# Performance work log

Hardware: AMD Instinct MI355X
Metric: run time of the kernel (lower is better)

## Reference

```python
import jax, jax.numpy as jnp
import numpy as np

NUM_EMBEDDINGS = 1024
EMBEDDING_DIM = 256
COMMITMENT_COST = 0.25


def setup_inputs() -> dict:
    key = jax.random.key(0)
    k1, k2 = jax.random.split(key)
    inputs = jax.random.normal(k1, (64, 1024, EMBEDDING_DIM), dtype=jnp.float32)
    # codebook initialized uniform(-1/K, 1/K) as in the torch module
    embedding = jax.random.uniform(
        k2, (NUM_EMBEDDINGS, EMBEDDING_DIM), dtype=jnp.float32,
        minval=-1.0 / NUM_EMBEDDINGS, maxval=1.0 / NUM_EMBEDDINGS)
    return {"inputs": inputs, "embedding": embedding}


def reference(inputs, embedding):
    # flatten to [N, D]
    D = embedding.shape[1]
    flat = inputs.reshape(-1, D)
    distances = (jnp.sum(flat * flat, axis=1, keepdims=True)
                 + jnp.sum(embedding * embedding, axis=1)
                 - 2.0 * jnp.matmul(flat, embedding.T))
    encoding_indices = jnp.argmin(distances, axis=1)  # [N]
    # one_hot @ embedding == gather; use gather (same math, no NxK one-hot)
    quantized = jnp.take(embedding, encoding_indices, axis=0).reshape(inputs.shape)
    # commitment loss: mse(stop_grad(quantized), inputs)
    e_latent_loss = jnp.mean(jnp.square(jax.lax.stop_gradient(quantized) - inputs))
    loss = COMMITMENT_COST * e_latent_loss
    # straight-through estimator
    quantized = inputs + jax.lax.stop_gradient(quantized - inputs)
    return quantized, loss, encoding_indices.reshape(inputs.shape[:-1])
```

## Files before the change

### kernel.cpp

```cpp
#include <hip/hip_runtime.h>
#include <cfloat>
#include <climits>

#define N_ROWS 65536
#define DIM 256
#define K_CODES 1024
#define N_ELEM 16777216
#define OUT_LOSS_OFF 16777216
#define OUT_IDX_OFF  16777217

#define ROWS_PB 128
#define CT 128
#define EPS_MARGIN 1.5e-4f
#define SHORTLIST_EPS 6e-4f
#define RB 8

#define WS_PARTIALS 0
#define WS_ESQ      8192
#define WS_IDX      12288
#define WS_FLAGCNT  274432
#define WS_FLAGLIST 274436
#define WS_EHI      540672
#define WS_ELO      1064960
#define WS_EHIT     1589248

typedef unsigned short u16;
typedef __attribute__((ext_vector_type(8))) short bf16x8;
typedef __attribute__((ext_vector_type(4))) float f32x4;

__device__ __forceinline__ void glds16(const u16* g, u16* l) {
    __builtin_amdgcn_global_load_lds(
        (const __attribute__((address_space(1))) unsigned int*)(const void*)g,
        (__attribute__((address_space(3))) unsigned int*)(void*)l,
        16, 0, 0);
}

__device__ __forceinline__ void bsplit(float x, u16& h, u16& l) {
    unsigned u = __float_as_uint(x);
    unsigned hb = (u + 0x7fffu + ((u >> 16) & 1u)) >> 16;
    h = (u16)hb;
    float hf = __uint_as_float(hb << 16);
    float lf = x - hf;
    unsigned u2 = __float_as_uint(lf);
    l = (u16)((u2 + 0x7fffu + ((u2 >> 16) & 1u)) >> 16);
}

__device__ __forceinline__ float np_pairwise_sumsq(const float* __restrict__ a) {
    float half[2];
    #pragma unroll
    for (int h = 0; h < 2; ++h) {
        const float* p = a + h * 128;
        float r[8];
        #pragma unroll
        for (int j = 0; j < 8; ++j) r[j] = __fmul_rn(p[j], p[j]);
        for (int i = 8; i < 128; i += 8) {
            #pragma unroll
            for (int j = 0; j < 8; ++j)
                r[j] = __fadd_rn(r[j], __fmul_rn(p[i + j], p[i + j]));
        }
        half[h] = __fadd_rn(__fadd_rn(__fadd_rn(r[0], r[1]), __fadd_rn(r[2], r[3])),
                            __fadd_rn(__fadd_rn(r[4], r[5]), __fadd_rn(r[6], r[7])));
    }
    return __fadd_rn(half[0], half[1]);
}

__global__ void xsplit_kernel(const float* __restrict__ x, u16* __restrict__ xhi,
                              u16* __restrict__ xlo) {
    int i4 = blockIdx.x * 256 + threadIdx.x;
    float4 v = ((const float4*)x)[i4];
    ushort4 h, l;
    bsplit(v.x, h.x, l.x); bsplit(v.y, h.y, l.y);
    bsplit(v.z, h.z, l.z); bsplit(v.w, h.w, l.w);
    ((ushort4*)xhi)[i4] = h;
    ((ushort4*)xlo)[i4] = l;
}

__global__ void esplit_kernel(const float* __restrict__ e, u16* __restrict__ ehi,
                              u16* __restrict__ elo, u16* __restrict__ ehiT) {
    int i4 = blockIdx.x * 256 + threadIdx.x;
    float4 v = ((const float4*)e)[i4];
    ushort4 h, l;
    bsplit(v.x, h.x, l.x); bsplit(v.y, h.y, l.y);
    bsplit(v.z, h.z, l.z); bsplit(v.w, h.w, l.w);
    ((ushort4*)ehi)[i4] = h;
    ((ushort4*)elo)[i4] = l;
    int c = i4 >> 6;
    int f4 = i4 & 63;
    int qid = f4 >> 1;
    ((ushort4*)ehiT)[((size_t)qid * 1024 + c) * 2 + (f4 & 1)] = h;
}

__global__ void esq_kernel(const float* __restrict__ e, float* __restrict__ esq) {
    int c = blockIdx.x * 256 + threadIdx.x;
    if (c < K_CODES) esq[c] = np_pairwise_sumsq(e + c * DIM);
}

__launch_bounds__(512, 4)
__global__ void argmin_kernel(const u16* __restrict__ xhi, const u16* __restrict__ xlo,
                              const u16* __restrict__ ehi, const u16* __restrict__ elo,
                              const float* __restrict__ esq, int* __restrict__ wsIdx,
                              int* __restrict__ flagCnt, int* __restrict__ flagList) {
    __shared__ __align__(16) unsigned char lds[65536];
    __shared__ float esq_s[CT];
    u16* xhiS = (u16*)lds;
    u16* xloS = (u16*)(lds + 16384);
    u16* ehiS = (u16*)(lds + 32768);
    u16* eloS = (u16*)(lds + 49152);

    const int t = threadIdx.x;
    const int w = t >> 6;
    const int l = t & 63;
    const int lane15 = l & 15;
    const int quad = l >> 4;
    const int rowBase = blockIdx.x * ROWS_PB;
    const int wr = w >> 1;
    const int wc = w & 1;

    float bv[8], sv[8]; int bi[8];
    #pragma unroll
    for (int i = 0; i < 8; ++i) { bv[i] = FLT_MAX; sv[i] = FLT_MAX; bi[i] = INT_MAX; }

    const int arr = w & 3;
    const int half = w >> 2;
    const u16* src; u16* dst; int gIsX;
    if (arr == 0)      { src = xhi; dst = xhiS; gIsX = 1; }
    else if (arr == 1) { src = xlo; dst = xloS; gIsX = 1; }
    else if (arr == 2) { src = ehi; dst = ehiS; gIsX = 0; }
    else               { src = elo; dst = eloS; gIsX = 0; }
    const int sub = l >> 3;
    const int jb = l & 7;
    const int sb = jb ^ sub;

    for (int ct = 0; ct < 8; ++ct) {
        const int ctBase = ct * CT;
        __syncthreads();
        if (t < CT) esq_s[t] = esq[ctBase + t];

        f32x4 acc[2][4];
        #pragma unroll
        for (int ti = 0; ti < 2; ++ti)
            #pragma unroll
            for (int tj = 0; tj < 4; ++tj) acc[ti][tj] = (f32x4){0.f, 0.f, 0.f, 0.f};

        for (int ch = 0; ch < 4; ++ch) {
            __syncthreads();
            const int gRowBase = gIsX ? rowBase : ctBase;
            #pragma unroll
            for (int i = 0; i < 8; ++i) {
                int r = half * 64 + i * 8 + sub;
                glds16(src + (size_t)(gRowBase + r) * 256 + ch * 64 + sb * 8,
                       dst + half * 4096 + i * 512);
            }
            __syncthreads();

            #pragma unroll
            for (int kk = 0; kk < 2; ++kk) {
                bf16x8 ah[2], al4[2], bh[4], bl[4];
                const int blk = kk * 4 + quad;
                #pragma unroll
                for (int ti = 0; ti < 2; ++ti) {
                    int r = wr * 32 + ti * 16 + lane15;
                    int off = r * 64 + ((blk ^ (r & 7)) * 8);
                    ah[ti]  = *(const bf16x8*)(xhiS + off);
                    al4[ti] = *(const bf16x8*)(xloS + off);
                }
                #pragma unroll
                for (int tj = 0; tj < 4; ++tj) {
                    int r = wc * 64 + tj * 16 + lane15;
                    int off = r * 64 + ((blk ^ (r & 7)) * 8);
                    bh[tj] = *(const bf16x8*)(ehiS + off);
                    bl[tj] = *(const bf16x8*)(eloS + off);
                }
                #pragma unroll
                for (int ti = 0; ti < 2; ++ti)
                    #pragma unroll
                    for (int tj = 0; tj < 4; ++tj) {
                        acc[ti][tj] = __builtin_amdgcn_mfma_f32_16x16x32_bf16(al4[ti], bh[tj], acc[ti][tj], 0, 0, 0);
                        acc[ti][tj] = __builtin_amdgcn_mfma_f32_16x16x32_bf16(ah[ti], bl[tj], acc[ti][tj], 0, 0, 0);
                        acc[ti][tj] = __builtin_amdgcn_mfma_f32_16x16x32_bf16(ah[ti], bh[tj], acc[ti][tj], 0, 0, 0);
                    }
            }
        }

        #pragma unroll
        for (int tj = 0; tj < 4; ++tj) {
            int cLoc = wc * 64 + tj * 16 + lane15;
            float cs = esq_s[cLoc];
            int c = ctBase + cLoc;
            #pragma unroll
            for (int ti = 0; ti < 2; ++ti)
                #pragma unroll
                for (int r4 = 0; r4 < 4; ++r4) {
                    int slot = ti * 4 + r4;
                    float s = fmaf(-2.0f, acc[ti][tj][r4], cs);
                    if (s < bv[slot]) {
                        sv[slot] = bv[slot]; bv[slot] = s; bi[slot] = c;
                    } else if (s < sv[slot]) {
                        sv[slot] = s;
                    }
                }
        }
    }

    __syncthreads();
    float* bvA = (float*)lds;
    float* svA = (float*)(lds + 16896);
    int*   biA = (int*)(lds + 33792);
    const int contrib = wc * 16 + lane15;
    #pragma unroll
    for (int slot = 0; slot < 8; ++slot) {
        int m = wr * 32 + (slot >> 2) * 16 + quad * 4 + (slot & 3);
        bvA[m * 33 + contrib] = bv[slot];
        svA[m * 33 + contrib] = sv[slot];
        biA[m * 33 + contrib] = bi[slot];
    }
    __syncthreads();

    if (t < ROWS_PB) {
        float bb = FLT_MAX, ss = FLT_MAX;
        int ii = INT_MAX;
        for (int k = 0; k < 32; ++k) {
            float v  = bvA[t * 33 + k];
            int   id = biA[t * 33 + k];
            float s2 = svA[t * 33 + k];
            if (v < bb || (v == bb && id < ii)) {
                ss = fminf(bb, s2);
                bb = v; ii = id;
            } else {
                ss = fminf(ss, v);
            }
        }
        int row = rowBase + t;
        wsIdx[row] = ii;
        if (ss - bb < EPS_MARGIN) {
            int p = atomicAdd(flagCnt, 1);
            flagList[p] = row;
        }
    }
}

__launch_bounds__(256)
__global__ void rescore_kernel(const float* __restrict__ x, const float* __restrict__ e,
                               const u16* __restrict__ ehiT, const float* __restrict__ esq,
                               int* __restrict__ wsIdx, const int* __restrict__ flagCnt,
                               const int* __restrict__ flagList) {
    __shared__ __align__(16) float xsh[RB][DIM];
    __shared__ float Ash[RB];
    __shared__ float minsh[RB][256];
    __shared__ float thrsh[RB];
    __shared__ int scnt[RB];
    __shared__ int slist[RB][32];
    __shared__ float sres[RB][32];
    const int t = threadIdx.x;
    const int cnt = *flagCnt;
    const int ngroups = (cnt + RB - 1) / RB;
    for (int g = blockIdx.x; g < ngroups; g += gridDim.x) {
        const int base = g * RB;
        const int nr = (cnt - base < RB) ? (cnt - base) : RB;
        __syncthreads();
        #pragma unroll
        for (int r = 0; r < RB; ++r)
            xsh[r][t] = (r < nr) ? x[(size_t)flagList[base + r] * DIM + t] : 0.0f;
        if (t < RB) scnt[t] = 0;
        __syncthreads();
        if (t < RB) Ash[t] = np_pairwise_sumsq(xsh[t]);

        float sA[4][RB];
        #pragma unroll
        for (int j = 0; j < 4; ++j)
            #pragma unroll
            for (int r = 0; r < RB; ++r) sA[j][r] = 0.0f;

        const uint4* eT4 = (const uint4*)ehiT;
        for (int q = 0; q < 32; ++q) {
            float4 xq[RB][2];
            #pragma unroll
            for (int r = 0; r < RB; ++r) {
                xq[r][0] = ((const float4*)xsh[r])[2 * q];
                xq[r][1] = ((const float4*)xsh[r])[2 * q + 1];
            }
            #pragma unroll
            for (int j = 0; j < 4; ++j) {
                uint4 uv = eT4[(size_t)q * 1024 + j * 256 + t];
                float e0 = __uint_as_float(uv.x << 16);
                float e1 = __uint_as_float(uv.x & 0xffff0000u);
                float e2 = __uint_as_float(uv.y << 16);
                float e3 = __uint_as_float(uv.y & 0xffff0000u);
                float e4v = __uint_as_float(uv.z << 16);
                float e5 = __uint_as_float(uv.z & 0xffff0000u);
                float e6 = __uint_as_float(uv.w << 16);
                float e7 = __uint_as_float(uv.w & 0xffff0000u);
                #pragma unroll
                for (int r = 0; r < RB; ++r) {
                    float d0 = sA[j][r];
                    d0 = fmaf(e0, xq[r][0].x, d0);
                    d0 = fmaf(e1, xq[r][0].y, d0);
                    d0 = fmaf(e2, xq[r][0].z, d0);
                    d0 = fmaf(e3, xq[r][0].w, d0);
                    d0 = fmaf(e4v, xq[r][1].x, d0);
                    d0 = fmaf(e5, xq[r][1].y, d0);
                    d0 = fmaf(e6, xq[r][1].z, d0);
                    d0 = fmaf(e7, xq[r][1].w, d0);
                    sA[j][r] = d0;
                }
            }
        }
        #pragma unroll
        for (int j = 0; j < 4; ++j) {
            float cs = esq[j * 256 + t];
            #pragma unroll
            for (int r = 0; r < RB; ++r)
                sA[j][r] = fmaf(-2.0f, sA[j][r], cs);
        }
        #pragma unroll
        for (int r = 0; r < RB; ++r)
            minsh[r][t] = fminf(fminf(sA[0][r], sA[1][r]), fminf(sA[2][r], sA[3][r]));
        __syncthreads();
        for (int off = 128; off > 0; off >>= 1) {
            if (t < off) {
                #pragma unroll
                for (int r = 0; r < RB; ++r)
                    minsh[r][t] = fminf(minsh[r][t], minsh[r][t + off]);
            }
            __syncthreads();
        }
        if (t < RB) thrsh[t] = minsh[t][0] + SHORTLIST_EPS;
        __syncthreads();
        #pragma unroll
        for (int j = 0; j < 4; ++j)
            #pragma unroll
            for (int r = 0; r < RB; ++r)
                if (r < nr && sA[j][r] <= thrsh[r]) {
                    int p = atomicAdd(&scnt[r], 1);
                    if (p < 32) slist[r][p] = j * 256 + t;
                }
        __syncthreads();
        {
            int r = t >> 5, k = t & 31;
            int ns = scnt[r] < 32 ? scnt[r] : 32;
            if (r < nr && k < ns) {
                int c = slist[r][k];
                const float4* ec4 = (const float4*)(e + (size_t)c * DIM);
                const float4* xc4 = (const float4*)xsh[r];
                double dot = 0.0;
                #pragma unroll 8
                for (int d4 = 0; d4 < 64; ++d4) {
                    float4 ev = ec4[d4];
                    float4 xv = xc4[d4];
                    dot += (double)ev.x * (double)xv.x + (double)ev.y * (double)xv.y
                         + (double)ev.z * (double)xv.z + (double)ev.w * (double)xv.w;
                }
                float M = (float)dot;
                sres[r][k] = __fsub_rn(__fadd_rn(Ash[r], esq[c]), __fmul_rn(2.0f, M));
            }
        }
        __syncthreads();
        if (t < nr) {
            int ns = scnt[t] < 32 ? scnt[t] : 32;
            float bb = FLT_MAX; int ii = INT_MAX;
            for (int k = 0; k < ns; ++k) {
                float s = sres[t][k]; int c = slist[t][k];
                if (s < bb || (s == bb && c < ii)) { bb = s; ii = c; }
            }
            wsIdx[flagList[base + t]] = ii;
        }
    }
}

__global__ void gather_kernel(const float* __restrict__ x, const float* __restrict__ e,
                              const int* __restrict__ wsIdx, float* __restrict__ out,
                              double* __restrict__ partials) {
    const float4* x4 = (const float4*)x;
    const float4* e4 = (const float4*)e;
    float4* q4 = (float4*)out;
    float* outIdx = out + OUT_IDX_OFF;
    const int tid = blockIdx.x * 256 + threadIdx.x;
    double sse = 0.0;
    #pragma unroll 4
    for (int i = 0; i < 16; ++i) {
        int u = tid + i * 262144;
        int row = u >> 6;
        int c4 = u & 63;
        int idx = wsIdx[row];
        float4 q = e4[idx * 64 + c4];
        float4 xv = x4[u];
        q4[u] = q;
        double dx = (double)q.x - (double)xv.x;
        double dy = (double)q.y - (double)xv.y;
        double dz = (double)q.z - (double)xv.z;
        double dw = (double)q.w - (double)xv.w;
        sse += dx * dx + dy * dy + dz * dz + dw * dw;
    }
    if (tid < N_ROWS) outIdx[tid] = (float)wsIdx[tid];
    #pragma unroll
    for (int m = 1; m < 64; m <<= 1) sse += __shfl_xor(sse, m);
    __shared__ double wsum[4];
    if ((threadIdx.x & 63) == 0) wsum[threadIdx.x >> 6] = sse;
    __syncthreads();
    if (threadIdx.x == 0)
        partials[blockIdx.x] = wsum[0] + wsum[1] + wsum[2] + wsum[3];
}

__global__ void loss_kernel(const double* __restrict__ partials, float* __restrict__ out) {
    __shared__ double sh[256];
    const int t = threadIdx.x;
    double s = partials[t] + partials[t + 256] + partials[t + 512] + partials[t + 768];
    sh[t] = s;
    __syncthreads();
    for (int off = 128; off > 0; off >>= 1) {
        if (t < off) sh[t] += sh[t + off];
        __syncthreads();
    }
    if (t == 0) out[OUT_LOSS_OFF] = (float)(0.25 * sh[0] / (double)N_ELEM);
}

extern "C" void kernel_launch(void* const* d_in, const int* in_sizes, int n_in,
                              void* d_out, int out_size, void* d_ws, size_t ws_size,
                              hipStream_t stream) {
    (void)in_sizes; (void)n_in; (void)out_size; (void)ws_size;
    const float* x = (const float*)d_in[0];
    const float* e = (const float*)d_in[1];
    float* out = (float*)d_out;
    char* ws = (char*)d_ws;
    double* partials = (double*)(ws + WS_PARTIALS);
    float* esq = (float*)(ws + WS_ESQ);
    int* wsIdx = (int*)(ws + WS_IDX);
    int* flagCnt = (int*)(ws + WS_FLAGCNT);
    int* flagList = (int*)(ws + WS_FLAGLIST);
    u16* ehi = (u16*)(ws + WS_EHI);
    u16* elo = (u16*)(ws + WS_ELO);
    u16* ehiT = (u16*)(ws + WS_EHIT);
    u16* xhi = (u16*)d_out;
    u16* xlo = xhi + N_ELEM;

    hipMemsetAsync(flagCnt, 0, sizeof(int), stream);
    xsplit_kernel<<<16384, 256, 0, stream>>>(x, xhi, xlo);
    esplit_kernel<<<256, 256, 0, stream>>>(e, ehi, elo, ehiT);
    esq_kernel<<<4, 256, 0, stream>>>(e, esq);
    argmin_kernel<<<N_ROWS / ROWS_PB, 512, 0, stream>>>(xhi, xlo, ehi, elo, esq,
                                                        wsIdx, flagCnt, flagList);
    rescore_kernel<<<512, 256, 0, stream>>>(x, e, ehiT, esq, wsIdx, flagCnt, flagList);
    gather_kernel<<<1024, 256, 0, stream>>>(x, e, wsIdx, out, partials);
    loss_kernel<<<1, 256, 0, stream>>>(partials, out);
}
```

Baseline: 321.5 us.

## Double-buffer LDS staging in argmin kernel to overlap loads with MFMA

Flattens the code-tile and K-chunk loops into one 32-step loop and double-buffers the shared-memory tiles, so the global-to-LDS copy for the next step is issued before the MFMAs on the current buffer. This cuts the barriers per step from two to one and preloads all code norms into LDS once. In exchange LDS per block doubles to 128 KB and the launch bound drops from 4 to 2 blocks per CU, which lowers occupancy.

```diff
diff --git a/kernel.cpp b/kernel.cpp
--- a/kernel.cpp
+++ b/kernel.cpp
@@ -95,17 +95,14 @@
     if (c < K_CODES) esq[c] = np_pairwise_sumsq(e + c * DIM);
 }
 
-__launch_bounds__(512, 4)
+__launch_bounds__(512, 2)
 __global__ void argmin_kernel(const u16* __restrict__ xhi, const u16* __restrict__ xlo,
                               const u16* __restrict__ ehi, const u16* __restrict__ elo,
                               const float* __restrict__ esq, int* __restrict__ wsIdx,
                               int* __restrict__ flagCnt, int* __restrict__ flagList) {
-    __shared__ __align__(16) unsigned char lds[65536];
-    __shared__ float esq_s[CT];
-    u16* xhiS = (u16*)lds;
-    u16* xloS = (u16*)(lds + 16384);
-    u16* ehiS = (u16*)(lds + 32768);
-    u16* eloS = (u16*)(lds + 49152);
+    __shared__ __align__(16) unsigned char lds[131072];
+    __shared__ float esqAll[K_CODES];
+    u16* ldsU = (u16*)lds;
 
     const int t = threadIdx.x;
     const int w = t >> 6;
@@ -122,87 +119,102 @@
 
     const int arr = w & 3;
     const int half = w >> 2;
-    const u16* src; u16* dst; int gIsX;
-    if (arr == 0)      { src = xhi; dst = xhiS; gIsX = 1; }
-    else if (arr == 1) { src = xlo; dst = xloS; gIsX = 1; }
-    else if (arr == 2) { src = ehi; dst = ehiS; gIsX = 0; }
-    else               { src = elo; dst = eloS; gIsX = 0; }
+    const u16* src; int gIsX;
+    if (arr == 0)      { src = xhi; gIsX = 1; }
+    else if (arr == 1) { src = xlo; gIsX = 1; }
+    else if (arr == 2) { src = ehi; gIsX = 0; }
+    else               { src = elo; gIsX = 0; }
+    const int dstOff = arr * 8192;
     const int sub = l >> 3;
     const int jb = l & 7;
     const int sb = jb ^ sub;
 
-    for (int ct = 0; ct < 8; ++ct) {
-        const int ctBase = ct * CT;
-        __syncthreads();
-        if (t < CT) esq_s[t] = esq[ctBase + t];
-
-        f32x4 acc[2][4];
-        #pragma unroll
-        for (int ti = 0; ti < 2; ++ti)
-            #pragma unroll
-            for (int tj = 0; tj < 4; ++tj) acc[ti][tj] = (f32x4){0.f, 0.f, 0.f, 0.f};
-
-        for (int ch = 0; ch < 4; ++ch) {
-            __syncthreads();
-            const int gRowBase = gIsX ? rowBase : ctBase;
-            #pragma unroll
-            for (int i = 0; i < 8; ++i) {
-                int r = half * 64 + i * 8 + sub;
-                glds16(src + (size_t)(gRowBase + r) * 256 + ch * 64 + sb * 8,
-                       dst + half * 4096 + i * 512);
-            }
-            __syncthreads();
-
-            #pragma unroll
-            for (int kk = 0; kk < 2; ++kk) {
-                bf16x8 ah[2], al4[2], bh[4], bl[4];
-                const int blk = kk * 4 + quad;
+    auto stageStep = [&](int s, int buf) {
+        const int ch = s & 3;
+        const int gRowBase = gIsX ? rowBase : (s >> 2) * CT;
+        u16* base = ldsU + buf * 32768 + dstOff + half * 4096;
+        #pragma unroll
+        for (int i = 0; i < 8; ++i) {
+            int r = half * 64 + i * 8 + sub;
+            glds16(src + (size_t)(gRowBase + r) * 256 + ch * 64 + sb * 8,
+                   base + i * 512);
+        }
+    };
+
+    esqAll[t] = esq[t];
+    esqAll[t + 512] = esq[t + 512];
+    stageStep(0, 0);
+    __syncthreads();
+
+    f32x4 acc[2][4];
+    int cur = 0;
+    for (int s = 0; s < 32; ++s) {
+        if ((s & 3) == 0) {
+            #pragma unroll
+            for (int ti = 0; ti < 2; ++ti)
                 #pragma unroll
-                for (int ti = 0; ti < 2; ++ti) {
-                    int r = wr * 32 + ti * 16 + lane15;
-                    int off = r * 64 + ((blk ^ (r & 7)) * 8);
-                    ah[ti]  = *(const bf16x8*)(xhiS + off);
-                    al4[ti] = *(const bf16x8*)(xloS + off);
-                }
+                for (int tj = 0; tj < 4; ++tj) acc[ti][tj] = (f32x4){0.f, 0.f, 0.f, 0.f};
+        }
+        if (s < 31) stageStep(s + 1, cur ^ 1);
+
+        const u16* xhiC = ldsU + cur * 32768;
+        const u16* xloC = xhiC + 8192;
+        const u16* ehiC = xhiC + 16384;
+        const u16* eloC = xhiC + 24576;
+
+        #pragma unroll
+        for (int kk = 0; kk < 2; ++kk) {
+            bf16x8 ah[2], al4[2], bh[4], bl[4];
+            const int blk = kk * 4 + quad;
+            #pragma unroll
+            for (int ti = 0; ti < 2; ++ti) {
+                int r = wr * 32 + ti * 16 + lane15;
+                int off = r * 64 + ((blk ^ (r & 7)) * 8);
+                ah[ti]  = *(const bf16x8*)(xhiC + off);
+                al4[ti] = *(const bf16x8*)(xloC + off);
+            }
+            #pragma unroll
+            for (int tj = 0; tj < 4; ++tj) {
+                int r = wc * 64 + tj * 16 + lane15;
+                int off = r * 64 + ((blk ^ (r & 7)) * 8);
+                bh[tj] = *(const bf16x8*)(ehiC + off);
+                bl[tj] = *(const bf16x8*)(eloC + off);
+            }
+            #pragma unroll
+            for (int ti = 0; ti < 2; ++ti)
                 #pragma unroll
                 for (int tj = 0; tj < 4; ++tj) {
-                    int r = wc * 64 + tj * 16 + lane15;
-                    int off = r * 64 + ((blk ^ (r & 7)) * 8);
-                    bh[tj] = *(const bf16x8*)(ehiS + off);
-                    bl[tj] = *(const bf16x8*)(eloS + off);
+                    acc[ti][tj] = __builtin_amdgcn_mfma_f32_16x16x32_bf16(al4[ti], bh[tj], acc[ti][tj], 0, 0, 0);
+                    acc[ti][tj] = __builtin_amdgcn_mfma_f32_16x16x32_bf16(ah[ti], bl[tj], acc[ti][tj], 0, 0, 0);
+                    acc[ti][tj] = __builtin_amdgcn_mfma_f32_16x16x32_bf16(ah[ti], bh[tj], acc[ti][tj], 0, 0, 0);
                 }
+        }
+
+        if ((s & 3) == 3) {
+            const int ctBase = (s >> 2) * CT;
+            #pragma unroll
+            for (int tj = 0; tj < 4; ++tj) {
+                int cLoc = wc * 64 + tj * 16 + lane15;
+                int c = ctBase + cLoc;
+                float cs = esqAll[c];
                 #pragma unroll
                 for (int ti = 0; ti < 2; ++ti)
                     #pragma unroll
-                    for (int tj = 0; tj < 4; ++tj) {
-                        acc[ti][tj] = __builtin_amdgcn_mfma_f32_16x16x32_bf16(al4[ti], bh[tj], acc[ti][tj], 0, 0, 0);
-                        acc[ti][tj] = __builtin_amdgcn_mfma_f32_16x16x32_bf16(ah[ti], bl[tj], acc[ti][tj], 0, 0, 0);
-                        acc[ti][tj] = __builtin_amdgcn_mfma_f32_16x16x32_bf16(ah[ti], bh[tj], acc[ti][tj], 0, 0, 0);
+                    for (int r4 = 0; r4 < 4; ++r4) {
+                        int slot = ti * 4 + r4;
+                        float sc = fmaf(-2.0f, acc[ti][tj][r4], cs);
+                        if (sc < bv[slot]) {
+                            sv[slot] = bv[slot]; bv[slot] = sc; bi[slot] = c;
+                        } else if (sc < sv[slot]) {
+                            sv[slot] = sc;
+                        }
                     }
             }
         }
-
-        #pragma unroll
-        for (int tj = 0; tj < 4; ++tj) {
-            int cLoc = wc * 64 + tj * 16 + lane15;
-            float cs = esq_s[cLoc];
-            int c = ctBase + cLoc;
-            #pragma unroll
-            for (int ti = 0; ti < 2; ++ti)
-                #pragma unroll
-                for (int r4 = 0; r4 < 4; ++r4) {
-                    int slot = ti * 4 + r4;
-                    float s = fmaf(-2.0f, acc[ti][tj][r4], cs);
-                    if (s < bv[slot]) {
-                        sv[slot] = bv[slot]; bv[slot] = s; bi[slot] = c;
-                    } else if (s < sv[slot]) {
-                        sv[slot] = s;
-                    }
-                }
-        }
-    }
-
-    __syncthreads();
+        __syncthreads();
+        cur ^= 1;
+    }
+
     float* bvA = (float*)lds;
     float* svA = (float*)(lds + 16896);
     int*   biA = (int*)(lds + 33792);
```

After: 378.4 us. +17.7%, slower.

## Fuse x bf16 hi/lo split into argmin kernel, drop xsplit pass

Applied to the files above, without the earlier changes.

Drops the separate xsplit kernel, which wrote bf16 hi/lo copies of the 64MB input to global memory. The argmin kernel now loads fp32 x tiles straight into LDS with an XOR swizzle. Each wave splits its fragments into hi/lo bf16 in registers using v_cvt_pk_bf16_f32. This removes a full read/write pass over the input, at the cost of recomputing the split for every codebook tile (8x per row block) and using more VALU in the MFMA loop.

```diff
diff --git a/kernel.cpp b/kernel.cpp
--- a/kernel.cpp
+++ b/kernel.cpp
@@ -27,12 +27,36 @@
 typedef unsigned short u16;
 typedef __attribute__((ext_vector_type(8))) short bf16x8;
 typedef __attribute__((ext_vector_type(4))) float f32x4;
-
-__device__ __forceinline__ void glds16(const u16* g, u16* l) {
+typedef union { bf16x8 v; unsigned u[4]; } frag_u;
+
+__device__ __forceinline__ void glds16(const void* g, void* l) {
     __builtin_amdgcn_global_load_lds(
-        (const __attribute__((address_space(1))) unsigned int*)(const void*)g,
-        (__attribute__((address_space(3))) unsigned int*)(void*)l,
+        (const __attribute__((address_space(1))) unsigned int*)g,
+        (__attribute__((address_space(3))) unsigned int*)l,
         16, 0, 0);
+}
+
+__device__ __forceinline__ unsigned cvt_pk_bf16(float lo, float hi) {
+    unsigned r;
+    asm("v_cvt_pk_bf16_f32 %0, %1, %2" : "=v"(r) : "v"(lo), "v"(hi));
+    return r;
+}
+
+__device__ __forceinline__ void split8(float4 a, float4 b, bf16x8& h8, bf16x8& l8) {
+    frag_u H, L;
+    float f0 = a.x, f1 = a.y, f2 = a.z, f3 = a.w;
+    float f4 = b.x, f5 = b.y, f6 = b.z, f7 = b.w;
+    const float* f[8] = {&f0,&f1,&f2,&f3,&f4,&f5,&f6,&f7};
+    #pragma unroll
+    for (int p = 0; p < 4; ++p) {
+        float xl = *f[2*p], xh = *f[2*p+1];
+        unsigned hw = cvt_pk_bf16(xl, xh);
+        float hfl = __uint_as_float(hw << 16);
+        float hfh = __uint_as_float(hw & 0xffff0000u);
+        H.u[p] = hw;
+        L.u[p] = cvt_pk_bf16(xl - hfl, xh - hfh);
+    }
+    h8 = H.v; l8 = L.v;
 }
 
 __device__ __forceinline__ void bsplit(float x, u16& h, u16& l) {
@@ -62,17 +86,6 @@
                             __fadd_rn(__fadd_rn(r[4], r[5]), __fadd_rn(r[6], r[7])));
     }
     return __fadd_rn(half[0], half[1]);
-}
-
-__global__ void xsplit_kernel(const float* __restrict__ x, u16* __restrict__ xhi,
-                              u16* __restrict__ xlo) {
-    int i4 = blockIdx.x * 256 + threadIdx.x;
-    float4 v = ((const float4*)x)[i4];
-    ushort4 h, l;
-    bsplit(v.x, h.x, l.x); bsplit(v.y, h.y, l.y);
-    bsplit(v.z, h.z, l.z); bsplit(v.w, h.w, l.w);
-    ((ushort4*)xhi)[i4] = h;
-    ((ushort4*)xlo)[i4] = l;
 }
 
 __global__ void esplit_kernel(const float* __restrict__ e, u16* __restrict__ ehi,
@@ -96,14 +109,13 @@
 }
 
 __launch_bounds__(512, 4)
-__global__ void argmin_kernel(const u16* __restrict__ xhi, const u16* __restrict__ xlo,
+__global__ void argmin_kernel(const float* __restrict__ x,
                               const u16* __restrict__ ehi, const u16* __restrict__ elo,
                               const float* __restrict__ esq, int* __restrict__ wsIdx,
                               int* __restrict__ flagCnt, int* __restrict__ flagList) {
     __shared__ __align__(16) unsigned char lds[65536];
     __shared__ float esq_s[CT];
-    u16* xhiS = (u16*)lds;
-    u16* xloS = (u16*)(lds + 16384);
+    float* xSf  = (float*)lds;
     u16* ehiS = (u16*)(lds + 32768);
     u16* eloS = (u16*)(lds + 49152);
 
@@ -120,16 +132,14 @@
     #pragma unroll
     for (int i = 0; i < 8; ++i) { bv[i] = FLT_MAX; sv[i] = FLT_MAX; bi[i] = INT_MAX; }
 
-    const int arr = w & 3;
-    const int half = w >> 2;
-    const u16* src; u16* dst; int gIsX;
-    if (arr == 0)      { src = xhi; dst = xhiS; gIsX = 1; }
-    else if (arr == 1) { src = xlo; dst = xloS; gIsX = 1; }
-    else if (arr == 2) { src = ehi; dst = ehiS; gIsX = 0; }
-    else               { src = elo; dst = eloS; gIsX = 0; }
-    const int sub = l >> 3;
-    const int jb = l & 7;
-    const int sb = jb ^ sub;
+    const int sub4 = l >> 4;
+    const int jb16 = l & 15;
+    const int sub8 = l >> 3;
+    const int jb8 = l & 7;
+    const int sb8 = jb8 ^ sub8;
+    const u16* srcE = (w < 6) ? ehi : elo;
+    u16* dstE = (w < 6) ? ehiS : eloS;
+    const int halfE = w & 1;
 
     for (int ct = 0; ct < 8; ++ct) {
         const int ctBase = ct * CT;
@@ -144,12 +154,21 @@
 
         for (int ch = 0; ch < 4; ++ch) {
             __syncthreads();
-            const int gRowBase = gIsX ? rowBase : ctBase;
-            #pragma unroll
-            for (int i = 0; i < 8; ++i) {
-                int r = half * 64 + i * 8 + sub;
-                glds16(src + (size_t)(gRowBase + r) * 256 + ch * 64 + sb * 8,
-                       dst + half * 4096 + i * 512);
+            if (w < 4) {
+                #pragma unroll
+                for (int i = 0; i < 8; ++i) {
+                    int r = w * 32 + i * 4 + sub4;
+                    int sbx = jb16 ^ (r & 15);
+                    glds16(x + (size_t)(rowBase + r) * 256 + ch * 64 + sbx * 4,
+                           (unsigned char*)lds + (w * 8 + i) * 1024);
+                }
+            } else {
+                #pragma unroll
+                for (int i = 0; i < 8; ++i) {
+                    int r = halfE * 64 + i * 8 + sub8;
+                    glds16(srcE + (size_t)(ctBase + r) * 256 + ch * 64 + sb8 * 8,
+                           dstE + halfE * 4096 + i * 512);
+                }
             }
             __syncthreads();
 
@@ -160,9 +179,12 @@
                 #pragma unroll
                 for (int ti = 0; ti < 2; ++ti) {
                     int r = wr * 32 + ti * 16 + lane15;
-                    int off = r * 64 + ((blk ^ (r & 7)) * 8);
-                    ah[ti]  = *(const bf16x8*)(xhiS + off);
-                    al4[ti] = *(const bf16x8*)(xloS + off);
+                    int base = r * 64;
+                    int s0 = ((2 * blk) ^ (r & 15)) * 4;
+                    int s1 = ((2 * blk + 1) ^ (r & 15)) * 4;
+                    float4 va = *(const float4*)(xSf + base + s0);
+                    float4 vb = *(const float4*)(xSf + base + s1);
+                    split8(va, vb, ah[ti], al4[ti]);
                 }
                 #pragma unroll
                 for (int tj = 0; tj < 4; ++tj) {
@@ -430,14 +452,11 @@
     u16* ehi = (u16*)(ws + WS_EHI);
     u16* elo = (u16*)(ws + WS_ELO);
     u16* ehiT = (u16*)(ws + WS_EHIT);
-    u16* xhi = (u16*)d_out;
-    u16* xlo = xhi + N_ELEM;
 
     hipMemsetAsync(flagCnt, 0, sizeof(int), stream);
-    xsplit_kernel<<<16384, 256, 0, stream>>>(x, xhi, xlo);
     esplit_kernel<<<256, 256, 0, stream>>>(e, ehi, elo, ehiT);
     esq_kernel<<<4, 256, 0, stream>>>(e, esq);
-    argmin_kernel<<<N_ROWS / ROWS_PB, 512, 0, stream>>>(xhi, xlo, ehi, elo, esq,
+    argmin_kernel<<<N_ROWS / ROWS_PB, 512, 0, stream>>>(x, ehi, elo, esq,
                                                         wsIdx, flagCnt, flagList);
     rescore_kernel<<<512, 256, 0, stream>>>(x, e, ehiT, esq, wsIdx, flagCnt, flagList);
     gather_kernel<<<1024, 256, 0, stream>>>(x, e, wsIdx, out, partials);
```

Measured after the change: 313.7 us. 1.02x faster.
